# Kernel tuning notes

Hardware: AMD Instinct MI355X
Metric: run time of the kernel (lower is better)

## Reference

```python
import jax, jax.numpy as jnp
import numpy as np

SUBSTEP = 10
FRAMES = 24
T = FRAMES * SUBSTEP
DT = 1.0 / 60.0 / SUBSTEP
SLOPE_DEG = 20.0
COS_S = float(np.cos(np.deg2rad(SLOPE_DEG)))
SIN_S = float(np.sin(np.deg2rad(SLOPE_DEG)))
INIT_HEIGHT = 0.1
N_VERTS = 2_000_000
GRAVITY = jnp.array([0.0, -9.8, 0.0], dtype=jnp.float32)
CONTACT_N = jnp.array([-SIN_S, COS_S, 0.0], dtype=jnp.float32)
EPS = 1e-6


def quat_mul(a, b):
    w1, x1, y1, z1 = a[0], a[1], a[2], a[3]
    w2, x2, y2, z2 = b[0], b[1], b[2], b[3]
    return jnp.stack([
        w1 * w2 - x1 * x2 - y1 * y2 - z1 * z2,
        w1 * x2 + x1 * w2 + y1 * z2 - z1 * y2,
        w1 * y2 + y1 * w2 + z1 * x2 - x1 * z2,
        w1 * z2 + z1 * w2 + x1 * y2 - y1 * x2,
    ])


def quat_to_matrix(q):
    q = q / jnp.linalg.norm(q)
    w, x, y, z = q[0], q[1], q[2], q[3]
    return jnp.stack([
        jnp.stack([1 - 2 * y * y - 2 * z * z, 2 * x * y - 2 * w * z, 2 * x * z + 2 * w * y]),
        jnp.stack([2 * x * y + 2 * w * z, 1 - 2 * x * x - 2 * z * z, 2 * y * z - 2 * w * x]),
        jnp.stack([2 * x * z - 2 * w * y, 2 * y * z + 2 * w * x, 1 - 2 * x * x - 2 * y * y]),
    ])


def cross_matrix(a):
    z = jnp.zeros((), dtype=a.dtype)
    return jnp.stack([
        jnp.stack([z, -a[2], a[1]]),
        jnp.stack([a[2], z, -a[0]]),
        jnp.stack([-a[1], a[0], z]),
    ])


def setup_inputs() -> dict:
    key = jax.random.key(0)
    k1, k2, k3 = jax.random.split(key, 3)
    return {
        "x": jax.random.normal(k1, (N_VERTS, 3), dtype=jnp.float32) * 0.2,
        "mass_center": jnp.zeros((3,), dtype=jnp.float32),
        "init_trans": jax.random.normal(k2, (3,), dtype=jnp.float32) * 0.3 + jnp.array([0.3, 0.5, 0.0]),
        "init_quat": jnp.ones((4,), dtype=jnp.float32),
        "init_v": jax.random.normal(k3, (3,), dtype=jnp.float32) * 0.1,
        "kn": jnp.array([0.5], dtype=jnp.float32),
        "mu": jnp.array([0.4], dtype=jnp.float32),
        "linear_damping": jnp.array([0.999], dtype=jnp.float32),
        "angular_damping": jnp.array([0.998], dtype=jnp.float32),
    }


def _simulate(x, mass_center, init_trans, init_quat, init_v, kn, mu, linear_damping, angular_damping):
    n = x.shape[0]
    mass = jnp.asarray(float(n), dtype=x.dtype)  # unit mass per vertex
    inv_mass = 1.0 / mass
    r = x - mass_center
    # inertia_reference = sum_i m*( (r.r) I - outer(r,r) )
    inertia = jnp.sum(jnp.einsum('ni,ni->n', r, r)) * jnp.eye(3, dtype=x.dtype) - jnp.einsum('ni,nj->ij', r, r)
    kn0, mu0 = kn[0], mu[0]
    ld, ad = linear_damping[0], angular_damping[0]
    eye3 = jnp.eye(3, dtype=x.dtype)

    def step(carry, _):
        trans, quat, v, omega = carry
        Rm = quat_to_matrix(quat)
        Rx = x @ Rm.T                                   # [N,3]
        xi = trans + Rx + mass_center                   # world positions
        vi_all = v + jnp.cross(omega[None, :], Rx)      # per-vertex velocities
        d = xi @ CONTACT_N
        rel_v = vi_all @ CONTACT_N
        mask = (d < -COS_S * INIT_HEIGHT) & (rel_v < 0.0)
        num = jnp.sum(mask)
        numf = jnp.maximum(num, 1).astype(x.dtype)
        sum_pos = jnp.sum(x * mask[:, None].astype(x.dtype), axis=0)
        ri = sum_pos / numf
        Ri = Rm @ ri
        vi = v + jnp.cross(omega, Ri)
        v_n = jnp.dot(vi, CONTACT_N) * CONTACT_N
        v_t = vi - v_n
        vn_new = -kn0 * v_n
        alpha = jnp.maximum(1.0 - mu0 * (1.0 + kn0) * (jnp.linalg.norm(v_n) / (jnp.linalg.norm(v_t) + EPS)), 0.0)
        vi_new = vn_new + alpha * v_t
        I = Rm @ inertia @ Rm.T
        I_inv = jnp.linalg.inv(I)
        Rri = cross_matrix(Ri)
        kmat = inv_mass * eye3 - Rri @ I_inv @ Rri
        J = jnp.linalg.solve(kmat, vi_new - vi)
        hit = num > 0
        dv = jnp.where(hit, J * inv_mass, 0.0)
        domega = jnp.where(hit, I_inv @ Rri @ J, 0.0)
        v_new = (v + GRAVITY * DT) * ld + dv
        omega_new = omega * ad + domega
        trans_new = trans + DT * v_new
        wq = jnp.concatenate([jnp.zeros((1,), dtype=x.dtype), omega_new]) * (0.5 * DT)
        quat_new = quat + quat_mul(wq, quat)
        quat_new = quat_new / jnp.linalg.norm(quat_new)
        new_carry = (trans_new, quat_new, v_new, omega_new)
        return new_carry, jnp.concatenate([trans_new, quat_new])

    carry0 = (init_trans, init_quat / jnp.linalg.norm(init_quat), init_v, jnp.zeros(3, dtype=x.dtype))
    _, traj = jax.lax.scan(step, carry0, None, length=T)
    return traj  # [T, 7] = translation(3) + quaternion(4) per substep


def reference(x, mass_center, init_trans, init_quat, init_v, kn, mu, linear_damping, angular_damping):
    return _simulate(x, mass_center, init_trans, init_quat, init_v, kn, mu, linear_damping, angular_damping)
```

## Files before the change

### kernel.cpp

```cpp
#include <hip/hip_runtime.h>

#define GRID   256
#define BLOCK  512
#define NWAVES (BLOCK / 64)
#define CHUNK  7813
#define SLOTS  16
#define NREPT  64

typedef unsigned long long u64;

__device__ __forceinline__ u64 rec_load(const u64* p) {
  return __hip_atomic_load(p, __ATOMIC_RELAXED, __HIP_MEMORY_SCOPE_AGENT);
}
__device__ __forceinline__ void rec_store(u64* p, u64 v) {
  __hip_atomic_store(p, v, __ATOMIC_RELAXED, __HIP_MEMORY_SCOPE_AGENT);
}
__device__ __forceinline__ u64 rec_pack(float f, unsigned tag) {
  return (u64)__float_as_uint(f) | ((u64)tag << 32);
}

#define C_NX   ((float)(-0.3420201433256687))
#define C_NY   ((float)( 0.9396926207859084))
#define C_DTF  ((float)(1.0 / 60.0 / 10.0))
#define C_HDT  ((float)(0.5 * (1.0 / 60.0 / 10.0)))
#define C_DTH  ((float)(-0.9396926207859084 * 0.1))
#define C_GYDT (-9.8f * (float)(1.0 / 60.0 / 10.0))

__device__ __forceinline__ void mat3_mul(const float* A, const float* B, float* C) {
  #pragma unroll
  for (int i = 0; i < 3; ++i)
    #pragma unroll
    for (int j = 0; j < 3; ++j)
      C[i*3+j] = A[i*3+0]*B[0*3+j] + A[i*3+1]*B[1*3+j] + A[i*3+2]*B[2*3+j];
}
__device__ __forceinline__ void mat3_mul_bt(const float* A, const float* B, float* C) {
  #pragma unroll
  for (int i = 0; i < 3; ++i)
    #pragma unroll
    for (int j = 0; j < 3; ++j)
      C[i*3+j] = A[i*3+0]*B[j*3+0] + A[i*3+1]*B[j*3+1] + A[i*3+2]*B[j*3+2];
}
__device__ __forceinline__ void mat3_inv(const float* m, float* inv) {
  float A =  (m[4]*m[8] - m[5]*m[7]);
  float B = -(m[3]*m[8] - m[5]*m[6]);
  float C =  (m[3]*m[7] - m[4]*m[6]);
  float det = m[0]*A + m[1]*B + m[2]*C;
  float id = 1.0f / det;
  inv[0] = A * id;
  inv[1] = -(m[1]*m[8] - m[2]*m[7]) * id;
  inv[2] =  (m[1]*m[5] - m[2]*m[4]) * id;
  inv[3] = B * id;
  inv[4] =  (m[0]*m[8] - m[2]*m[6]) * id;
  inv[5] = -(m[0]*m[5] - m[2]*m[3]) * id;
  inv[6] = C * id;
  inv[7] = -(m[0]*m[7] - m[1]*m[6]) * id;
  inv[8] =  (m[0]*m[4] - m[1]*m[3]) * id;
}

__global__ __launch_bounds__(BLOCK, 2)
void sim_kernel(const float* __restrict__ xg,
                const float* __restrict__ mc_p,
                const float* __restrict__ itr_p,
                const float* __restrict__ iq_p,
                const float* __restrict__ iv_p,
                const float* __restrict__ kn_p,
                const float* __restrict__ mu_p,
                const float* __restrict__ ldp_p,
                const float* __restrict__ adp_p,
                float* __restrict__ out,
                u64* __restrict__ ws,
                int N, int T)
{
  const int tid  = threadIdx.x;
  const int bid  = blockIdx.x;
  const int lane = tid & 63;
  const int wid  = tid >> 6;

  __shared__ float s_redI[NWAVES * 6];
  __shared__ float s_red[2][NWAVES * 4];
  __shared__ float s_gat[NWAVES * 4];

  u64* part = ws;
  u64* tot  = ws + 2 * 4 * GRID;
  u64* bufI = ws + 2 * 4 * GRID + 2 * NREPT * 4;

  const float mc0 = mc_p[0], mc1 = mc_p[1], mc2 = mc_p[2];

  const int vstart = bid * CHUNK;
  int cl = N - vstart; if (cl > CHUNK) cl = CHUNK; if (cl < 0) cl = 0;

  const float NANF = __int_as_float(0x7fc00000);
  float xr0[SLOTS], xr1[SLOTS], xr2[SLOTS];
  #pragma unroll
  for (int s = 0; s < SLOTS; ++s) {
    const int i = tid + s * BLOCK;
    if (i < cl) {
      const float* p = xg + (size_t)(vstart + i) * 3;
      xr0[s] = p[0]; xr1[s] = p[1]; xr2[s] = p[2];
    } else {
      xr0[s] = NANF; xr1[s] = NANF; xr2[s] = NANF;
    }
  }

  {
    float v6[6] = {0,0,0,0,0,0};
    #pragma unroll
    for (int s = 0; s < SLOTS; ++s) {
      if (tid + s * BLOCK < cl) {
        float r0 = xr0[s] - mc0, r1 = xr1[s] - mc1, r2 = xr2[s] - mc2;
        v6[0] += r0*r0; v6[1] += r1*r1; v6[2] += r2*r2;
        v6[3] += r0*r1; v6[4] += r0*r2; v6[5] += r1*r2;
      }
    }
    #pragma unroll
    for (int off = 32; off > 0; off >>= 1)
      #pragma unroll
      for (int k = 0; k < 6; ++k) v6[k] += __shfl_down(v6[k], off, 64);
    if (lane == 0) {
      #pragma unroll
      for (int k = 0; k < 6; ++k) s_redI[wid * 6 + k] = v6[k];
    }
    __syncthreads();
    if (tid == 0) {
      float t6[6];
      #pragma unroll
      for (int k = 0; k < 6; ++k) {
        t6[k] = s_redI[k];
        #pragma unroll
        for (int w = 1; w < NWAVES; ++w) t6[k] += s_redI[w * 6 + k];
      }
      #pragma unroll
      for (int k = 0; k < 6; ++k) rec_store(bufI + k * GRID + bid, rec_pack(t6[k], 0xC0FFEEu));
    }
    __syncthreads();
  }

  float In[9];
  {
    float g6[6] = {0,0,0,0,0,0};
    if (tid < GRID) {
      u64 r[6];
      int f = 0;
      for (;;) {
        #pragma unroll
        for (int k = 0; k < 6; ++k) r[k] = rec_load(bufI + k * GRID + tid);
        bool ok = true;
        #pragma unroll
        for (int k = 0; k < 6; ++k) ok &= ((unsigned)(r[k] >> 32) == 0xC0FFEEu);
        if (ok) break;
        if ((++f & 15) == 0) __builtin_amdgcn_s_sleep(1);
      }
      #pragma unroll
      for (int k = 0; k < 6; ++k) g6[k] = __uint_as_float((unsigned)r[k]);
    }
    #pragma unroll
    for (int off = 32; off > 0; off >>= 1)
      #pragma unroll
      for (int k = 0; k < 6; ++k) g6[k] += __shfl_down(g6[k], off, 64);
    if (lane == 0) {
      #pragma unroll
      for (int k = 0; k < 6; ++k) s_redI[wid * 6 + k] = g6[k];
    }
    __syncthreads();
    float t6[6];
    #pragma unroll
    for (int k = 0; k < 6; ++k) {
      t6[k] = s_redI[k];
      #pragma unroll
      for (int w = 1; w < NWAVES; ++w) t6[k] += s_redI[w * 6 + k];
    }
    float trc = t6[0] + t6[1] + t6[2];
    In[0] = trc - t6[0]; In[4] = trc - t6[1]; In[8] = trc - t6[2];
    In[1] = -t6[3]; In[3] = -t6[3];
    In[2] = -t6[4]; In[6] = -t6[4];
    In[5] = -t6[5]; In[7] = -t6[5];
  }

  float tr0 = itr_p[0], tr1 = itr_p[1], tr2 = itr_p[2];
  float q0 = iq_p[0], q1 = iq_p[1], q2 = iq_p[2], q3 = iq_p[3];
  {
    float n0 = sqrtf(q0*q0 + q1*q1 + q2*q2 + q3*q3);
    q0 /= n0; q1 /= n0; q2 /= n0; q3 /= n0;
  }
  float v0 = iv_p[0], v1 = iv_p[1], v2 = iv_p[2];
  float om0 = 0.f, om1 = 0.f, om2 = 0.f;
  const float knv = kn_p[0], muv = mu_p[0], ldv = ldp_p[0], adv = adp_p[0];
  const float inv_mass = 1.0f / (float)N;

  float Rm[9], Ii[9];
  float pa0, pa1, pa2, pb0, pb1, pb2, pca, pcb;
  int skip;

  {
    float qn = sqrtf(q0*q0 + q1*q1 + q2*q2 + q3*q3);
    float w = q0/qn, xq = q1/qn, yq = q2/qn, zq = q3/qn;
    Rm[0] = 1.f - 2.f*yq*yq - 2.f*zq*zq; Rm[1] = 2.f*xq*yq - 2.f*w*zq; Rm[2] = 2.f*xq*zq + 2.f*w*yq;
    Rm[3] = 2.f*xq*yq + 2.f*w*zq; Rm[4] = 1.f - 2.f*xq*xq - 2.f*zq*zq; Rm[5] = 2.f*yq*zq - 2.f*w*xq;
    Rm[6] = 2.f*xq*zq - 2.f*w*yq; Rm[7] = 2.f*yq*zq + 2.f*w*xq; Rm[8] = 1.f - 2.f*xq*xq - 2.f*yq*yq;
    pa0 = Rm[0]*C_NX + Rm[3]*C_NY;
    pa1 = Rm[1]*C_NX + Rm[4]*C_NY;
    pa2 = Rm[2]*C_NX + Rm[5]*C_NY;
    float w0 = C_NY*om2, w1 = -C_NX*om2, w2 = C_NX*om1 - C_NY*om0;
    pb0 = Rm[0]*w0 + Rm[3]*w1 + Rm[6]*w2;
    pb1 = Rm[1]*w0 + Rm[4]*w1 + Rm[7]*w2;
    pb2 = Rm[2]*w0 + Rm[5]*w1 + Rm[8]*w2;
    pca = C_DTH - ((tr0 + mc0)*C_NX + (tr1 + mc1)*C_NY);
    pcb = -(v0*C_NX + v1*C_NY);
    skip = (om0 == 0.f && om1 == 0.f && om2 == 0.f && !(pcb > 0.f)) ? 1 : 0;
    float Tm[9]; mat3_mul(Rm, In, Tm);
    float Iw[9]; mat3_mul_bt(Tm, Rm, Iw);
    mat3_inv(Iw, Ii);
  }

  int pub = 0;
  for (int t = 0; t < T; ++t) {
    float tn = 0.f, tx = 0.f, ty = 0.f, tz = 0.f;

    if (!skip) {
      const int p = pub & 1;
      const unsigned want = (unsigned)(pub + 1);

      float acc0 = 0.f, acc1 = 0.f, acc2 = 0.f, acc3 = 0.f;
      #pragma unroll
      for (int s = 0; s < SLOTS; ++s) {
        const float x0 = xr0[s], x1 = xr1[s], x2 = xr2[s];
        const float da = x0*pa0 + x1*pa1 + x2*pa2;
        const float db = x0*pb0 + x1*pb1 + x2*pb2;
        if (da < pca && db < pcb) {
          acc0 += 1.f; acc1 += x0; acc2 += x1; acc3 += x2;
        }
      }
      #pragma unroll
      for (int off = 32; off > 0; off >>= 1) {
        acc0 += __shfl_down(acc0, off, 64);
        acc1 += __shfl_down(acc1, off, 64);
        acc2 += __shfl_down(acc2, off, 64);
        acc3 += __shfl_down(acc3, off, 64);
      }
      float* srA = s_red[p];
      if (lane == 0) {
        srA[wid*4+0] = acc0; srA[wid*4+1] = acc1;
        srA[wid*4+2] = acc2; srA[wid*4+3] = acc3;
      }
      __syncthreads();
      if (tid < 4) {
        float tw = srA[tid];
        #pragma unroll
        for (int w2 = 1; w2 < NWAVES; ++w2) tw += srA[w2*4 + tid];
        rec_store(part + (size_t)p * 4 * GRID + (size_t)tid * GRID + bid,
                  rec_pack(tw, want));
      }

      {
        float Tm[9]; mat3_mul(Rm, In, Tm);
        float Iw[9]; mat3_mul_bt(Tm, Rm, Iw);
        mat3_inv(Iw, Ii);
      }

      if (bid == 0) {
        float f0 = 0.f, f1 = 0.f, f2 = 0.f, f3 = 0.f;
        if (tid < GRID) {
          const u64* pp = part + (size_t)p * 4 * GRID + tid;
          u64 r0, r1, r2, r3;
          int fl = 0;
          for (;;) {
            r0 = rec_load(pp + 0 * GRID);
            r1 = rec_load(pp + 1 * GRID);
            r2 = rec_load(pp + 2 * GRID);
            r3 = rec_load(pp + 3 * GRID);
            if (((unsigned)(r0 >> 32) == want) && ((unsigned)(r1 >> 32) == want) &&
                ((unsigned)(r2 >> 32) == want) && ((unsigned)(r3 >> 32) == want)) break;
            if ((++fl & 15) == 0) __builtin_amdgcn_s_sleep(1);
          }
          f0 = __uint_as_float((unsigned)r0);
          f1 = __uint_as_float((unsigned)r1);
          f2 = __uint_as_float((unsigned)r2);
          f3 = __uint_as_float((unsigned)r3);
        }
        #pragma unroll
        for (int off = 32; off > 0; off >>= 1) {
          f0 += __shfl_down(f0, off, 64);
          f1 += __shfl_down(f1, off, 64);
          f2 += __shfl_down(f2, off, 64);
          f3 += __shfl_down(f3, off, 64);
        }
        if (lane == 0) {
          s_gat[wid*4+0] = f0; s_gat[wid*4+1] = f1;
          s_gat[wid*4+2] = f2; s_gat[wid*4+3] = f3;
        }
        __syncthreads();
        tn = s_gat[0]; tx = s_gat[1]; ty = s_gat[2]; tz = s_gat[3];
        #pragma unroll
        for (int w2 = 1; w2 < NWAVES; ++w2) {
          tn += s_gat[w2*4+0]; tx += s_gat[w2*4+1];
          ty += s_gat[w2*4+2]; tz += s_gat[w2*4+3];
        }
        if (tid < NREPT * 4) {
          const int w2 = tid & 3;
          const float val = (w2 == 0) ? tn : (w2 == 1) ? tx : (w2 == 2) ? ty : tz;
          rec_store(tot + (size_t)p * NREPT * 4 + tid, rec_pack(val, want));
        }
      } else {
        const u64* tp = tot + (size_t)p * NREPT * 4 + (size_t)(bid & (NREPT - 1)) * 4;
        u64 r0, r1, r2, r3;
        int fl = 0;
        for (;;) {
          r0 = rec_load(tp + 0); r1 = rec_load(tp + 1);
          r2 = rec_load(tp + 2); r3 = rec_load(tp + 3);
          if (((unsigned)(r0 >> 32) == want) && ((unsigned)(r1 >> 32) == want) &&
              ((unsigned)(r2 >> 32) == want) && ((unsigned)(r3 >> 32) == want)) break;
          if ((++fl & 31) == 0) __builtin_amdgcn_s_sleep(1);
        }
        tn = __uint_as_float((unsigned)r0);
        tx = __uint_as_float((unsigned)r1);
        ty = __uint_as_float((unsigned)r2);
        tz = __uint_as_float((unsigned)r3);
      }
      ++pub;
    }

    {
      float dv0 = 0.f, dv1 = 0.f, dv2 = 0.f, dm0 = 0.f, dm1 = 0.f, dm2 = 0.f;
      if (tn > 0.0f) {
        float numf = fmaxf(tn, 1.0f);
        float ri0 = tx/numf, ri1 = ty/numf, ri2 = tz/numf;
        float Ri0 = Rm[0]*ri0 + Rm[1]*ri1 + Rm[2]*ri2;
        float Ri1 = Rm[3]*ri0 + Rm[4]*ri1 + Rm[5]*ri2;
        float Ri2 = Rm[6]*ri0 + Rm[7]*ri1 + Rm[8]*ri2;
        float vi0 = v0 + om1*Ri2 - om2*Ri1;
        float vi1 = v1 + om2*Ri0 - om0*Ri2;
        float vi2 = v2 + om0*Ri1 - om1*Ri0;
        float vdn = vi0*C_NX + vi1*C_NY;
        float vn0 = vdn*C_NX, vn1 = vdn*C_NY;
        float vt0 = vi0 - vn0, vt1 = vi1 - vn1, vt2 = vi2;
        float nvn = sqrtf(vn0*vn0 + vn1*vn1);
        float nvt = sqrtf(vt0*vt0 + vt1*vt1 + vt2*vt2);
        float alpha = fmaxf(1.0f - muv*(1.0f + knv)*(nvn/(nvt + 1e-6f)), 0.0f);
        float dvi0 = (-knv*vn0 + alpha*vt0) - vi0;
        float dvi1 = (-knv*vn1 + alpha*vt1) - vi1;
        float dvi2 = (alpha*vt2) - vi2;
        float Cx[9] = {0.f, -Ri2, Ri1,  Ri2, 0.f, -Ri0,  -Ri1, Ri0, 0.f};
        float T2[9]; mat3_mul(Cx, Ii, T2);
        float T3[9]; mat3_mul(T2, Cx, T3);
        float Km[9];
        #pragma unroll
        for (int m = 0; m < 9; ++m) Km[m] = -T3[m];
        Km[0] += inv_mass; Km[4] += inv_mass; Km[8] += inv_mass;
        float Ki[9]; mat3_inv(Km, Ki);
        float J0 = Ki[0]*dvi0 + Ki[1]*dvi1 + Ki[2]*dvi2;
        float J1 = Ki[3]*dvi0 + Ki[4]*dvi1 + Ki[5]*dvi2;
        float J2 = Ki[6]*dvi0 + Ki[7]*dvi1 + Ki[8]*dvi2;
        dv0 = J0*inv_mass; dv1 = J1*inv_mass; dv2 = J2*inv_mass;
        float c0 = -Ri2*J1 + Ri1*J2;
        float c1 =  Ri2*J0 - Ri0*J2;
        float c2 = -Ri1*J0 + Ri0*J1;
        dm0 = Ii[0]*c0 + Ii[1]*c1 + Ii[2]*c2;
        dm1 = Ii[3]*c0 + Ii[4]*c1 + Ii[5]*c2;
        dm2 = Ii[6]*c0 + Ii[7]*c1 + Ii[8]*c2;
      }
      v0 = v0*ldv + dv0;
      v1 = (v1 + C_GYDT)*ldv + dv1;
      v2 = v2*ldv + dv2;
      om0 = om0*adv + dm0; om1 = om1*adv + dm1; om2 = om2*adv + dm2;
      tr0 += C_DTF*v0; tr1 += C_DTF*v1; tr2 += C_DTF*v2;
      float wx = om0*C_HDT, wy = om1*C_HDT, wz = om2*C_HDT;
      float dq0 = -wx*q1 - wy*q2 - wz*q3;
      float dq1 =  wx*q0 + wy*q3 - wz*q2;
      float dq2 =  wy*q0 + wz*q1 - wx*q3;
      float dq3 =  wz*q0 + wx*q2 - wy*q1;
      q0 += dq0; q1 += dq1; q2 += dq2; q3 += dq3;
      float qn2 = sqrtf(q0*q0 + q1*q1 + q2*q2 + q3*q3);
      q0 /= qn2; q1 /= qn2; q2 /= qn2; q3 /= qn2;
      if (bid == 0 && tid == 0) {
        float* o = out + (size_t)t * 7;
        o[0] = tr0; o[1] = tr1; o[2] = tr2;
        o[3] = q0;  o[4] = q1;  o[5] = q2;  o[6] = q3;
      }
      float qn = sqrtf(q0*q0 + q1*q1 + q2*q2 + q3*q3);
      float w = q0/qn, xq = q1/qn, yq = q2/qn, zq = q3/qn;
      Rm[0] = 1.f - 2.f*yq*yq - 2.f*zq*zq; Rm[1] = 2.f*xq*yq - 2.f*w*zq; Rm[2] = 2.f*xq*zq + 2.f*w*yq;
      Rm[3] = 2.f*xq*yq + 2.f*w*zq; Rm[4] = 1.f - 2.f*xq*xq - 2.f*zq*zq; Rm[5] = 2.f*yq*zq - 2.f*w*xq;
      Rm[6] = 2.f*xq*zq - 2.f*w*yq; Rm[7] = 2.f*yq*zq + 2.f*w*xq; Rm[8] = 1.f - 2.f*xq*xq - 2.f*yq*yq;
      pa0 = Rm[0]*C_NX + Rm[3]*C_NY;
      pa1 = Rm[1]*C_NX + Rm[4]*C_NY;
      pa2 = Rm[2]*C_NX + Rm[5]*C_NY;
      float w0 = C_NY*om2, w1 = -C_NX*om2, w2 = C_NX*om1 - C_NY*om0;
      pb0 = Rm[0]*w0 + Rm[3]*w1 + Rm[6]*w2;
      pb1 = Rm[1]*w0 + Rm[4]*w1 + Rm[7]*w2;
      pb2 = Rm[2]*w0 + Rm[5]*w1 + Rm[8]*w2;
      pca = C_DTH - ((tr0 + mc0)*C_NX + (tr1 + mc1)*C_NY);
      pcb = -(v0*C_NX + v1*C_NY);
      skip = (om0 == 0.f && om1 == 0.f && om2 == 0.f && !(pcb > 0.f)) ? 1 : 0;
    }
  }
}

extern "C" void kernel_launch(void* const* d_in, const int* in_sizes, int n_in,
                              void* d_out, int out_size, void* d_ws, size_t ws_size,
                              hipStream_t stream) {
  const float* x   = (const float*)d_in[0];
  const float* mc  = (const float*)d_in[1];
  const float* itr = (const float*)d_in[2];
  const float* iq  = (const float*)d_in[3];
  const float* iv  = (const float*)d_in[4];
  const float* kn  = (const float*)d_in[5];
  const float* mu  = (const float*)d_in[6];
  const float* ldp = (const float*)d_in[7];
  const float* adp = (const float*)d_in[8];
  float* out = (float*)d_out;
  u64* ws  = (u64*)d_ws;
  int N = in_sizes[0] / 3;
  int T = out_size / 7;

  void* args[] = {(void*)&x, (void*)&mc, (void*)&itr, (void*)&iq, (void*)&iv,
                  (void*)&kn, (void*)&mu, (void*)&ldp, (void*)&adp,
                  (void*)&out, (void*)&ws, (void*)&N, (void*)&T};
  hipLaunchCooperativeKernel((void*)sim_kernel, dim3(GRID), dim3(BLOCK),
                             args, 0, stream);
}
```

Before: 1.430 ms.

## Replace tagged gather/broadcast reduction with fixed-point atomic accumulation and counter barrier

Each step's cross-block reduction now has every block atomically add fixed-point scaled partial sums into per-step global slots and bump an arrival counter. Each block then spins until the counter reaches the grid size and reads the totals directly. This replaces the two-hop scheme, where block 0 gathered tagged partials and rebroadcast them to replica slots, and the inertia reduction gets the same treatment. The aim is to cut per-step synchronisation latency. In exchange it adds a cooperative grid sync for zeroing, contention on a single atomic counter, and quantisation error from fixed-point accumulation.

```diff
diff --git a/kernel.cpp b/kernel.cpp
--- a/kernel.cpp
+++ b/kernel.cpp
@@ -1,23 +1,20 @@
 #include <hip/hip_runtime.h>
+#include <hip/hip_cooperative_groups.h>
 
 #define GRID   256
 #define BLOCK  512
 #define NWAVES (BLOCK / 64)
 #define CHUNK  7813
 #define SLOTS  16
-#define NREPT  64
 
 typedef unsigned long long u64;
-
-__device__ __forceinline__ u64 rec_load(const u64* p) {
-  return __hip_atomic_load(p, __ATOMIC_RELAXED, __HIP_MEMORY_SCOPE_AGENT);
-}
-__device__ __forceinline__ void rec_store(u64* p, u64 v) {
-  __hip_atomic_store(p, v, __ATOMIC_RELAXED, __HIP_MEMORY_SCOPE_AGENT);
-}
-__device__ __forceinline__ u64 rec_pack(float f, unsigned tag) {
-  return (u64)__float_as_uint(f) | ((u64)tag << 32);
-}
+typedef unsigned int u32;
+
+namespace cg = cooperative_groups;
+
+
+#define SCALEF   268435456.0f
+#define INV_SCALE (1.0 / 268435456.0)
 
 #define C_NX   ((float)(-0.3420201433256687))
 #define C_NY   ((float)( 0.9396926207859084))
@@ -25,6 +22,30 @@
 #define C_HDT  ((float)(0.5 * (1.0 / 60.0 / 10.0)))
 #define C_DTH  ((float)(-0.9396926207859084 * 0.1))
 #define C_GYDT (-9.8f * (float)(1.0 / 60.0 / 10.0))
+
+template <int NV>
+__device__ __forceinline__ void block_reduce(float* v, float* sm) {
+  #pragma unroll
+  for (int off = 32; off > 0; off >>= 1) {
+    #pragma unroll
+    for (int k = 0; k < NV; ++k) v[k] += __shfl_down(v[k], off, 64);
+  }
+  const int lane = threadIdx.x & 63;
+  const int wid  = threadIdx.x >> 6;
+  if (lane == 0) {
+    #pragma unroll
+    for (int k = 0; k < NV; ++k) sm[wid * NV + k] = v[k];
+  }
+  __syncthreads();
+  if (threadIdx.x == 0) {
+    #pragma unroll
+    for (int w = 1; w < NWAVES; ++w) {
+      #pragma unroll
+      for (int k = 0; k < NV; ++k) v[k] += sm[w * NV + k];
+    }
+  }
+  __syncthreads();
+}
 
 __device__ __forceinline__ void mat3_mul(const float* A, const float* B, float* C) {
   #pragma unroll
@@ -55,6 +76,13 @@
   inv[6] = C * id;
   inv[7] = -(m[0]*m[7] - m[1]*m[6]) * id;
   inv[8] =  (m[0]*m[4] - m[1]*m[3]) * id;
+}
+
+__device__ __forceinline__ u64 agent_load_u64(const u64* p) {
+  return __hip_atomic_load(p, __ATOMIC_RELAXED, __HIP_MEMORY_SCOPE_AGENT);
+}
+__device__ __forceinline__ u32 agent_load_u32(const u32* p) {
+  return __hip_atomic_load(p, __ATOMIC_RELAXED, __HIP_MEMORY_SCOPE_AGENT);
 }
 
 __global__ __launch_bounds__(BLOCK, 2)
@@ -77,12 +105,24 @@
   const int wid  = tid >> 6;
 
   __shared__ float s_redI[NWAVES * 6];
-  __shared__ float s_red[2][NWAVES * 4];
-  __shared__ float s_gat[NWAVES * 4];
-
-  u64* part = ws;
-  u64* tot  = ws + 2 * 4 * GRID;
-  u64* bufI = ws + 2 * 4 * GRID + 2 * NREPT * 4;
+  __shared__ float s_red[NWAVES * 4];
+  __shared__ float s_tot[4];
+  __shared__ float s_in[6];
+
+  u64* inb = ws + (size_t)256 * 48;
+
+  if (bid < T && tid < 5) {
+    u64* rb = ws + (size_t)bid * 48;
+    if (tid < 2)      __hip_atomic_store(rb + tid,      0ull, __ATOMIC_RELAXED, __HIP_MEMORY_SCOPE_AGENT);
+    else if (tid < 4) __hip_atomic_store(rb + 14 + tid, 0ull, __ATOMIC_RELAXED, __HIP_MEMORY_SCOPE_AGENT);
+    else              __hip_atomic_store((u32*)(rb + 32), 0u, __ATOMIC_RELAXED, __HIP_MEMORY_SCOPE_AGENT);
+  }
+  if (bid == GRID - 1 && tid < 7) {
+    if (tid < 3)      __hip_atomic_store(inb + tid,      0ull, __ATOMIC_RELAXED, __HIP_MEMORY_SCOPE_AGENT);
+    else if (tid < 6) __hip_atomic_store(inb + 13 + tid, 0ull, __ATOMIC_RELAXED, __HIP_MEMORY_SCOPE_AGENT);
+    else              __hip_atomic_store((u32*)(inb + 32), 0u, __ATOMIC_RELAXED, __HIP_MEMORY_SCOPE_AGENT);
+  }
+  cg::this_grid().sync();
 
   const float mc0 = mc_p[0], mc1 = mc_p[1], mc2 = mc_p[2];
 
@@ -112,68 +152,40 @@
         v6[3] += r0*r1; v6[4] += r0*r2; v6[5] += r1*r2;
       }
     }
-    #pragma unroll
-    for (int off = 32; off > 0; off >>= 1)
-      #pragma unroll
-      for (int k = 0; k < 6; ++k) v6[k] += __shfl_down(v6[k], off, 64);
-    if (lane == 0) {
-      #pragma unroll
-      for (int k = 0; k < 6; ++k) s_redI[wid * 6 + k] = v6[k];
+    block_reduce<6>(v6, s_redI);
+    if (tid == 0) {
+      atomicAdd(inb + 0,  (u64)(long long)__float2ll_rn(v6[0] * SCALEF));
+      atomicAdd(inb + 1,  (u64)(long long)__float2ll_rn(v6[1] * SCALEF));
+      atomicAdd(inb + 2,  (u64)(long long)__float2ll_rn(v6[2] * SCALEF));
+      atomicAdd(inb + 16, (u64)(long long)__float2ll_rn(v6[3] * SCALEF));
+      atomicAdd(inb + 17, (u64)(long long)__float2ll_rn(v6[4] * SCALEF));
+      atomicAdd(inb + 18, (u64)(long long)__float2ll_rn(v6[5] * SCALEF));
+      __builtin_amdgcn_fence(__ATOMIC_RELEASE, "agent");
+      atomicAdd((u32*)(inb + 32), 1u);
+      int f = 0;
+      for (;;) {
+        u32 c = agent_load_u32((u32*)(inb + 32));
+        if (c >= GRID) break;
+        if ((++f & 1) == 0) __builtin_amdgcn_s_sleep(1);
+      }
+      __builtin_amdgcn_fence(__ATOMIC_ACQUIRE, "agent");
+      s_in[0] = (float)((double)(long long)agent_load_u64(inb + 0)  * INV_SCALE);
+      s_in[1] = (float)((double)(long long)agent_load_u64(inb + 1)  * INV_SCALE);
+      s_in[2] = (float)((double)(long long)agent_load_u64(inb + 2)  * INV_SCALE);
+      s_in[3] = (float)((double)(long long)agent_load_u64(inb + 16) * INV_SCALE);
+      s_in[4] = (float)((double)(long long)agent_load_u64(inb + 17) * INV_SCALE);
+      s_in[5] = (float)((double)(long long)agent_load_u64(inb + 18) * INV_SCALE);
     }
     __syncthreads();
-    if (tid == 0) {
-      float t6[6];
-      #pragma unroll
-      for (int k = 0; k < 6; ++k) {
-        t6[k] = s_redI[k];
-        #pragma unroll
-        for (int w = 1; w < NWAVES; ++w) t6[k] += s_redI[w * 6 + k];
-      }
-      #pragma unroll
-      for (int k = 0; k < 6; ++k) rec_store(bufI + k * GRID + bid, rec_pack(t6[k], 0xC0FFEEu));
-    }
-    __syncthreads();
-  }
-
+  }
   float In[9];
   {
-    float g6[6] = {0,0,0,0,0,0};
-    if (tid < GRID) {
-      u64 r[6];
-      int f = 0;
-      for (;;) {
-        #pragma unroll
-        for (int k = 0; k < 6; ++k) r[k] = rec_load(bufI + k * GRID + tid);
-        bool ok = true;
-        #pragma unroll
-        for (int k = 0; k < 6; ++k) ok &= ((unsigned)(r[k] >> 32) == 0xC0FFEEu);
-        if (ok) break;
-        if ((++f & 15) == 0) __builtin_amdgcn_s_sleep(1);
-      }
-      #pragma unroll
-      for (int k = 0; k < 6; ++k) g6[k] = __uint_as_float((unsigned)r[k]);
-    }
-    #pragma unroll
-    for (int off = 32; off > 0; off >>= 1)
-      #pragma unroll
-      for (int k = 0; k < 6; ++k) g6[k] += __shfl_down(g6[k], off, 64);
-    if (lane == 0) {
-      #pragma unroll
-      for (int k = 0; k < 6; ++k) s_redI[wid * 6 + k] = g6[k];
-    }
-    __syncthreads();
-    float t6[6];
-    #pragma unroll
-    for (int k = 0; k < 6; ++k) {
-      t6[k] = s_redI[k];
-      #pragma unroll
-      for (int w = 1; w < NWAVES; ++w) t6[k] += s_redI[w * 6 + k];
-    }
-    float trc = t6[0] + t6[1] + t6[2];
-    In[0] = trc - t6[0]; In[4] = trc - t6[1]; In[8] = trc - t6[2];
-    In[1] = -t6[3]; In[3] = -t6[3];
-    In[2] = -t6[4]; In[6] = -t6[4];
-    In[5] = -t6[5]; In[7] = -t6[5];
+    float t0 = s_in[0], t1 = s_in[1], t2 = s_in[2];
+    float trc = t0 + t1 + t2;
+    In[0] = trc - t0; In[4] = trc - t1; In[8] = trc - t2;
+    In[1] = -s_in[3]; In[3] = -s_in[3];
+    In[2] = -s_in[4]; In[6] = -s_in[4];
+    In[5] = -s_in[5]; In[7] = -s_in[5];
   }
 
   float tr0 = itr_p[0], tr1 = itr_p[1], tr2 = itr_p[2];
@@ -212,13 +224,11 @@
     mat3_inv(Iw, Ii);
   }
 
-  int pub = 0;
   for (int t = 0; t < T; ++t) {
     float tn = 0.f, tx = 0.f, ty = 0.f, tz = 0.f;
 
     if (!skip) {
-      const int p = pub & 1;
-      const unsigned want = (unsigned)(pub + 1);
+      u64* rb = ws + (size_t)t * 48;
 
       float acc0 = 0.f, acc1 = 0.f, acc2 = 0.f, acc3 = 0.f;
       #pragma unroll
@@ -237,86 +247,41 @@
         acc2 += __shfl_down(acc2, off, 64);
         acc3 += __shfl_down(acc3, off, 64);
       }
-      float* srA = s_red[p];
       if (lane == 0) {
-        srA[wid*4+0] = acc0; srA[wid*4+1] = acc1;
-        srA[wid*4+2] = acc2; srA[wid*4+3] = acc3;
+        s_red[wid*4+0] = acc0; s_red[wid*4+1] = acc1;
+        s_red[wid*4+2] = acc2; s_red[wid*4+3] = acc3;
       }
       __syncthreads();
+
       if (tid < 4) {
-        float tw = srA[tid];
+        float tw = s_red[tid];
         #pragma unroll
-        for (int w2 = 1; w2 < NWAVES; ++w2) tw += srA[w2*4 + tid];
-        rec_store(part + (size_t)p * 4 * GRID + (size_t)tid * GRID + bid,
-                  rec_pack(tw, want));
-      }
-
-      {
-        float Tm[9]; mat3_mul(Rm, In, Tm);
-        float Iw[9]; mat3_mul_bt(Tm, Rm, Iw);
-        mat3_inv(Iw, Ii);
-      }
-
-      if (bid == 0) {
-        float f0 = 0.f, f1 = 0.f, f2 = 0.f, f3 = 0.f;
-        if (tid < GRID) {
-          const u64* pp = part + (size_t)p * 4 * GRID + tid;
-          u64 r0, r1, r2, r3;
-          int fl = 0;
-          for (;;) {
-            r0 = rec_load(pp + 0 * GRID);
-            r1 = rec_load(pp + 1 * GRID);
-            r2 = rec_load(pp + 2 * GRID);
-            r3 = rec_load(pp + 3 * GRID);
-            if (((unsigned)(r0 >> 32) == want) && ((unsigned)(r1 >> 32) == want) &&
-                ((unsigned)(r2 >> 32) == want) && ((unsigned)(r3 >> 32) == want)) break;
-            if ((++fl & 15) == 0) __builtin_amdgcn_s_sleep(1);
-          }
-          f0 = __uint_as_float((unsigned)r0);
-          f1 = __uint_as_float((unsigned)r1);
-          f2 = __uint_as_float((unsigned)r2);
-          f3 = __uint_as_float((unsigned)r3);
+        for (int w2 = 1; w2 < NWAVES; ++w2) tw += s_red[w2*4 + tid];
+        long long q = (tid == 0) ? (long long)tw : (long long)__float2ll_rn(tw * SCALEF);
+        u64* ap = rb + ((tid < 2) ? tid : 14 + tid);
+        atomicAdd(ap, (u64)q);
+      }
+      if (tid == 0) {
+        __builtin_amdgcn_fence(__ATOMIC_RELEASE, "agent");
+        atomicAdd((u32*)(rb + 32), 1u);
+        int f = 0;
+        for (;;) {
+          u32 c = agent_load_u32((u32*)(rb + 32));
+          if (c >= GRID) break;
+          if ((++f & 1) == 0) __builtin_amdgcn_s_sleep(1);
         }
-        #pragma unroll
-        for (int off = 32; off > 0; off >>= 1) {
-          f0 += __shfl_down(f0, off, 64);
-          f1 += __shfl_down(f1, off, 64);
-          f2 += __shfl_down(f2, off, 64);
-          f3 += __shfl_down(f3, off, 64);
-        }
-        if (lane == 0) {
-          s_gat[wid*4+0] = f0; s_gat[wid*4+1] = f1;
-          s_gat[wid*4+2] = f2; s_gat[wid*4+3] = f3;
-        }
-        __syncthreads();
-        tn = s_gat[0]; tx = s_gat[1]; ty = s_gat[2]; tz = s_gat[3];
-        #pragma unroll
-        for (int w2 = 1; w2 < NWAVES; ++w2) {
-          tn += s_gat[w2*4+0]; tx += s_gat[w2*4+1];
-          ty += s_gat[w2*4+2]; tz += s_gat[w2*4+3];
-        }
-        if (tid < NREPT * 4) {
-          const int w2 = tid & 3;
-          const float val = (w2 == 0) ? tn : (w2 == 1) ? tx : (w2 == 2) ? ty : tz;
-          rec_store(tot + (size_t)p * NREPT * 4 + tid, rec_pack(val, want));
-        }
-      } else {
-        const u64* tp = tot + (size_t)p * NREPT * 4 + (size_t)(bid & (NREPT - 1)) * 4;
-        u64 r0, r1, r2, r3;
-        int fl = 0;
-        for (;;) {
-          r0 = rec_load(tp + 0); r1 = rec_load(tp + 1);
-          r2 = rec_load(tp + 2); r3 = rec_load(tp + 3);
-          if (((unsigned)(r0 >> 32) == want) && ((unsigned)(r1 >> 32) == want) &&
-              ((unsigned)(r2 >> 32) == want) && ((unsigned)(r3 >> 32) == want)) break;
-          if ((++fl & 31) == 0) __builtin_amdgcn_s_sleep(1);
-        }
-        tn = __uint_as_float((unsigned)r0);
-        tx = __uint_as_float((unsigned)r1);
-        ty = __uint_as_float((unsigned)r2);
-        tz = __uint_as_float((unsigned)r3);
-      }
-      ++pub;
+        __builtin_amdgcn_fence(__ATOMIC_ACQUIRE, "agent");
+        u64 a0 = agent_load_u64(rb + 0);
+        u64 a1 = agent_load_u64(rb + 1);
+        u64 b0 = agent_load_u64(rb + 16);
+        u64 b1 = agent_load_u64(rb + 17);
+        s_tot[0] = (float)(long long)a0;
+        s_tot[1] = (float)((double)(long long)a1 * INV_SCALE);
+        s_tot[2] = (float)((double)(long long)b0 * INV_SCALE);
+        s_tot[3] = (float)((double)(long long)b1 * INV_SCALE);
+      }
+      __syncthreads();
+      tn = s_tot[0]; tx = s_tot[1]; ty = s_tot[2]; tz = s_tot[3];
     }
 
     {
@@ -391,6 +356,9 @@
       pca = C_DTH - ((tr0 + mc0)*C_NX + (tr1 + mc1)*C_NY);
       pcb = -(v0*C_NX + v1*C_NY);
       skip = (om0 == 0.f && om1 == 0.f && om2 == 0.f && !(pcb > 0.f)) ? 1 : 0;
+      float Tm[9]; mat3_mul(Rm, In, Tm);
+      float Iw[9]; mat3_mul_bt(Tm, Rm, Iw);
+      mat3_inv(Iw, Ii);
     }
   }
 }
```

New measurement: 3.610 ms. 152% more time.
